# Optimization experiments

Measured on AMD Instinct MI355X. Metric: run time of the kernel, lower is better.

The kernel has to match this reference:

```python
import jax, jax.numpy as jnp
import numpy as np

N, L, C, K = 8, 16384, 256, 64  # batch, points, d_color, anchor_num; d_struct = 4*K = 256


def setup_inputs() -> dict:
    key = jax.random.key(0)
    ks = jax.random.split(key, 12)
    d_in = C + 4 * K  # 512
    s1, s2, s3 = 1.0 / np.sqrt(d_in), 1.0 / np.sqrt(128), 1.0 / np.sqrt(256)
    return {
        'feat0': jax.random.normal(ks[0], (N, L, C), jnp.float32),
        'feat1': jax.random.normal(ks[1], (N, L, C), jnp.float32),
        'pts_3d0': jax.random.normal(ks[2], (N, L, 3), jnp.float32),
        'pts_3d1': jax.random.normal(ks[3], (N, L, 3), jnp.float32),
        'anchor_i': jax.random.randint(ks[4], (N, K), 0, L, jnp.int32),
        'anchor_j': jax.random.randint(ks[5], (N, K), 0, L, jnp.int32),
        'W1': jax.random.uniform(ks[6], (d_in, 128), jnp.float32, -s1, s1),
        'b1': jax.random.uniform(ks[7], (128,), jnp.float32, -s1, s1),
        'W2': jax.random.uniform(ks[8], (128, 256), jnp.float32, -s2, s2),
        'b2': jax.random.uniform(ks[9], (256,), jnp.float32, -s2, s2),
        'W3': jax.random.uniform(ks[10], (256, C), jnp.float32, -s3, s3),
        'b3': jax.random.uniform(ks[11], (C,), jnp.float32, -s3, s3),
    }


def _structured(pts, anchor_idx):
    # pts: [N,L,3], anchor_idx: [N,K] -> [N,L,4K]
    anchors = jnp.take_along_axis(pts, anchor_idx[:, :, None], axis=1)  # [N,K,3]
    diff = pts[:, :, None, :] - anchors[:, None, :, :]                  # [N,L,K,3]
    dist = jnp.sum(diff * diff, axis=-1, keepdims=True)                 # [N,L,K,1]
    f = jnp.concatenate([diff, dist], axis=-1)                          # [N,L,K,4]
    f = f / jnp.sum(jnp.abs(f), axis=-2, keepdims=True)                 # L1 norm over K
    f = jnp.swapaxes(f, -1, -2).reshape(pts.shape[0], pts.shape[1], -1)  # [N,L,4K]
    # original l1_norm is @torch.no_grad -> structured feature is detached
    return jax.lax.stop_gradient(f)


def _mlp(x, W1, b1, W2, b2, W3, b3):
    h = jax.nn.relu(x @ W1 + b1)
    h = jax.nn.relu(h @ W2 + b2)  # dropout is identity in eval
    return h @ W3 + b3


def reference(feat0, feat1, pts_3d0, pts_3d1, anchor_i, anchor_j,
              W1, b1, W2, b2, W3, b3):
    s0 = _structured(pts_3d0, anchor_i)
    s1 = _structured(pts_3d1, anchor_j)
    aug0 = _mlp(jnp.concatenate([feat0, s0], axis=-1), W1, b1, W2, b2, W3, b3)
    aug1 = _mlp(jnp.concatenate([feat1, s1], axis=-1), W1, b1, W2, b2, W3, b3)
    return aug0, aug1
```

## Files before the change

kernel.cpp:

```cpp
#include <hip/hip_runtime.h>

typedef __bf16 bf16x8 __attribute__((ext_vector_type(8)));
typedef float f32x4 __attribute__((ext_vector_type(4)));
typedef unsigned short u16x4 __attribute__((ext_vector_type(4)));

#define NBATCH 8
#define LPTS   16384
#define CDIM   256
#define KANC   64
#define DIN    512
#define H1DIM  128
#define H2DIM  256
#define TM     64

__device__ __forceinline__ unsigned short f2b(float f){
  __bf16 h = (__bf16)f;
  return __builtin_bit_cast(unsigned short, h);
}

#define LBAR() do{ \
  asm volatile("s_waitcnt lgkmcnt(0)" ::: "memory"); \
  __builtin_amdgcn_s_barrier(); \
  asm volatile("" ::: "memory"); \
} while(0)

__global__ __launch_bounds__(256) void prep_weights(
    const float* __restrict__ W1, const float* __restrict__ W2,
    const float* __restrict__ W3, unsigned short* __restrict__ wt){
  int id = blockIdx.x * 256 + threadIdx.x;
  if (id < 65536){
    int r = id >> 9, c = id & 511;
    wt[id] = f2b(W1[c * 128 + r]);
  } else if (id < 98304){
    int t = id - 65536; int r = t >> 7, c = t & 127;
    wt[id] = f2b(W2[c * 256 + r]);
  } else if (id < 163840){
    int t = id - 98304; int r = t >> 8, c = t & 255;
    wt[id] = f2b(W3[c * 256 + r]);
  }
}

__global__ __launch_bounds__(128) void prep_coef(
    const float* __restrict__ pts0, const float* __restrict__ pts1,
    const int* __restrict__ anc_i, const int* __restrict__ anc_j,
    const float* __restrict__ W1, float* __restrict__ coef){
  const int comb = blockIdx.x;
  const int strm = comb >> 3, n = comb & 7;
  const int col  = threadIdx.x;
  __shared__ float4 anc[64];
  const float* pts  = strm ? pts1 : pts0;
  const int*   anci = strm ? anc_j : anc_i;
  if (col < 64){
    int ai = anci[n * KANC + col];
    const float* ap = pts + ((size_t)n * LPTS + ai) * 3;
    anc[col] = make_float4(ap[0], ap[1], ap[2], 0.f);
  }
  __syncthreads();
  float SX=0,CX=0,SY=0,CY=0,SZ=0,CZ=0,SD=0,ADx=0,ADy=0,ADz=0,CD2=0;
  float SAx=0,SAy=0,SAz=0,SA2=0;
  for (int k = 0; k < KANC; ++k){
    float4 a = anc[k];
    float ak2 = a.x*a.x + a.y*a.y + a.z*a.z;
    float wx = W1[(256 + k) * 128 + col];
    float wy = W1[(320 + k) * 128 + col];
    float wz = W1[(384 + k) * 128 + col];
    float wd = W1[(448 + k) * 128 + col];
    SX += wx; CX += a.x * wx;
    SY += wy; CY += a.y * wy;
    SZ += wz; CZ += a.z * wz;
    SD += wd; ADx += a.x * wd; ADy += a.y * wd; ADz += a.z * wd;
    CD2 += ak2 * wd;
    SAx += a.x; SAy += a.y; SAz += a.z; SA2 += ak2;
  }
  float* cf = coef + (size_t)comb * 12 * 128;
  cf[ 0*128+col]=SX;  cf[ 1*128+col]=CX;  cf[ 2*128+col]=SY;  cf[ 3*128+col]=CY;
  cf[ 4*128+col]=SZ;  cf[ 5*128+col]=CZ;  cf[ 6*128+col]=SD;  cf[ 7*128+col]=ADx;
  cf[ 8*128+col]=ADy; cf[ 9*128+col]=ADz; cf[10*128+col]=CD2;
  if (col == 0) cf[11*128+0] = SAx;
  if (col == 1) cf[11*128+1] = SAy;
  if (col == 2) cf[11*128+2] = SAz;
  if (col == 3) cf[11*128+3] = SA2;
}

__global__ __launch_bounds__(512, 4) void fused(
    const float* __restrict__ feat0, const float* __restrict__ feat1,
    const float* __restrict__ pts0, const float* __restrict__ pts1,
    const int* __restrict__ anc_i, const int* __restrict__ anc_j,
    const float* __restrict__ b1, const float* __restrict__ b2,
    const float* __restrict__ b3, const unsigned short* __restrict__ wt,
    const float* __restrict__ coef, float* __restrict__ out)
{
  __shared__ unsigned short xs[TM * 256];
  __shared__ unsigned short h1s[TM * H1DIM];
  __shared__ float scal[TM][12];
  unsigned short* h2s = xs;

  const int tid  = threadIdx.x;
  const int wg   = blockIdx.x;
  const int strm = wg >> 11;
  const int n    = (wg >> 8) & 7;
  const int l0   = (wg & 255) * TM;

  const float* feat = strm ? feat1 : feat0;
  const float* pts  = strm ? pts1 : pts0;
  const int*   anci = strm ? anc_j : anc_i;
  const float* cf   = coef + (size_t)((strm << 3) | n) * 12 * 128;

  const int lane = tid & 63;
  const int w    = tid >> 6;
  const int lr   = lane & 15;
  const int lg   = lane >> 4;
  const int col1 = w * 16 + lr;
  const int col0 = w * 32;
  const unsigned short* wrow1 = wt + col1 * DIN;
  const unsigned short* w2t = wt + 65536;
  const unsigned short* w3t = wt + 98304;

  float ax, ay, az;
  {
    int ai = anci[n * KANC + lane];
    const float* ap = pts + ((size_t)n * LPTS + ai) * 3;
    ax = ap[0]; ay = ap[1]; az = ap[2];
  }
  const float* pp = pts + ((size_t)n * LPTS + l0 + (tid >> 3)) * 3;
  float px = pp[0], py = pp[1], pz = pp[2];
  float SAx = cf[11*128+0], SAy = cf[11*128+1], SAz = cf[11*128+2], SA2 = cf[11*128+3];
  float cc[11];
  #pragma unroll
  for (int j = 0; j < 11; ++j) cc[j] = cf[j * 128 + col1];
  float bias1 = b1[col1];

  {
    const float4* fb = (const float4*)(feat + ((size_t)n * LPTS + l0) * CDIM);
    #pragma unroll
    for (int it = 0; it < 8; ++it){
      int flat = it * 512 + tid;
      int r = flat >> 6, c4 = flat & 63;
      float4 v = fb[flat];
      int e = (r * 256 + c4 * 4) ^ ((r & 7) << 3);
      u16x4 pk = { f2b(v.x), f2b(v.y), f2b(v.z), f2b(v.w) };
      *(u16x4*)&xs[e] = pk;
    }
  }

  {
    const int l   = tid >> 3;
    const int sub = tid & 7;
    float s0 = 0.f, s1 = 0.f, s2 = 0.f;
    #pragma unroll
    for (int i = 0; i < 8; ++i){
      int src = sub * 8 + i;
      float akx = __shfl(ax, src, 64);
      float aky = __shfl(ay, src, 64);
      float akz = __shfl(az, src, 64);
      s0 += fabsf(px - akx); s1 += fabsf(py - aky); s2 += fabsf(pz - akz);
    }
    #pragma unroll
    for (int m = 1; m <= 4; m <<= 1){
      s0 += __shfl_xor(s0, m, 64);
      s1 += __shfl_xor(s1, m, 64);
      s2 += __shfl_xor(s2, m, 64);
    }
    float pp2 = px*px + py*py + pz*pz;
    float s3 = 64.f * pp2 - 2.f * (px*SAx + py*SAy + pz*SAz) + SA2;
    float i0 = 1.f/s0, i1 = 1.f/s1, i2 = 1.f/s2, i3 = 1.f/s3;
    float u;
    switch (sub){
      case 0: u = i0 * px;       break;
      case 1: u = -i0;           break;
      case 2: u = i1 * py;       break;
      case 3: u = -i1;           break;
      case 4: u = i2 * pz;       break;
      case 5: u = -i2;           break;
      case 6: u = i3 * pp2;      break;
      default: u = -2.f*i3*px;   break;
    }
    scal[l][sub] = u;
    if (sub < 3){
      float u2 = (sub == 0) ? -2.f*i3*py : (sub == 1) ? -2.f*i3*pz : i3;
      scal[l][8 + sub] = u2;
    }
  }

  bf16x8 b1b[8];
  #pragma unroll
  for (int kk = 0; kk < 8; ++kk)
    b1b[kk] = *(const bf16x8*)&wrow1[kk * 32 + lg * 8];

  LBAR();

  {
    f32x4 acc[4] = {};
    #pragma unroll
    for (int kk = 0; kk < 8; ++kk){
      int kb = kk * 32 + lg * 8;
      #pragma unroll
      for (int m = 0; m < 4; ++m){
        int row = m * 16 + lr;
        bf16x8 a = *(const bf16x8*)&xs[(row * 256 + kb) ^ ((row & 7) << 3)];
        acc[m] = __builtin_amdgcn_mfma_f32_16x16x32_bf16(a, b1b[kk], acc[m], 0, 0, 0);
      }
    }
    #pragma unroll
    for (int m = 0; m < 4; ++m){
      #pragma unroll
      for (int r = 0; r < 4; ++r){
        int row = m * 16 + lg * 4 + r;
        f32x4 ua = *(const f32x4*)&scal[row][0];
        f32x4 ub = *(const f32x4*)&scal[row][4];
        f32x4 uc = *(const f32x4*)&scal[row][8];
        float s = acc[m][r] + bias1;
        s += ua[0]*cc[0] + ua[1]*cc[1] + ua[2]*cc[2] + ua[3]*cc[3];
        s += ub[0]*cc[4] + ub[1]*cc[5] + ub[2]*cc[6] + ub[3]*cc[7];
        s += uc[0]*cc[8] + uc[1]*cc[9] + uc[2]*cc[10];
        float v = fmaxf(s, 0.f);
        h1s[(row * H1DIM + col1) ^ ((row & 7) << 3)] = f2b(v);
      }
    }
  }

  bf16x8 b2b[8];
  #pragma unroll
  for (int kk = 0; kk < 4; ++kk){
    int kb = kk * 32 + lg * 8;
    b2b[kk * 2    ] = *(const bf16x8*)&w2t[(col0      + lr) * H1DIM + kb];
    b2b[kk * 2 + 1] = *(const bf16x8*)&w2t[(col0 + 16 + lr) * H1DIM + kb];
  }

  LBAR();

  {
    f32x4 acc[4][2] = {};
    #pragma unroll
    for (int kk = 0; kk < 4; ++kk){
      int kb = kk * 32 + lg * 8;
      #pragma unroll
      for (int m = 0; m < 4; ++m){
        int row = m * 16 + lr;
        bf16x8 a = *(const bf16x8*)&h1s[(row * H1DIM + kb) ^ ((row & 7) << 3)];
        acc[m][0] = __builtin_amdgcn_mfma_f32_16x16x32_bf16(a, b2b[kk*2  ], acc[m][0], 0, 0, 0);
        acc[m][1] = __builtin_amdgcn_mfma_f32_16x16x32_bf16(a, b2b[kk*2+1], acc[m][1], 0, 0, 0);
      }
    }
    #pragma unroll
    for (int nt = 0; nt < 2; ++nt){
      int col = col0 + nt * 16 + lr;
      float bias = b2[col];
      #pragma unroll
      for (int m = 0; m < 4; ++m){
        #pragma unroll
        for (int r = 0; r < 4; ++r){
          int row = m * 16 + lg * 4 + r;
          float v = fmaxf(acc[m][nt][r] + bias, 0.f);
          h2s[(row * H2DIM + col) ^ ((row & 7) << 3)] = f2b(v);
        }
      }
    }
  }

  bf16x8 b3b[8];
  #pragma unroll
  for (int kk = 0; kk < 4; ++kk){
    int kb = kk * 32 + lg * 8;
    b3b[kk * 2    ] = *(const bf16x8*)&w3t[(col0      + lr) * H2DIM + kb];
    b3b[kk * 2 + 1] = *(const bf16x8*)&w3t[(col0 + 16 + lr) * H2DIM + kb];
  }

  LBAR();

  {
    f32x4 acc[4][2] = {};
    #pragma unroll
    for (int kk = 0; kk < 4; ++kk){
      int kb = kk * 32 + lg * 8;
      #pragma unroll
      for (int m = 0; m < 4; ++m){
        int row = m * 16 + lr;
        bf16x8 a = *(const bf16x8*)&h2s[(row * H2DIM + kb) ^ ((row & 7) << 3)];
        acc[m][0] = __builtin_amdgcn_mfma_f32_16x16x32_bf16(a, b3b[kk*2  ], acc[m][0], 0, 0, 0);
        acc[m][1] = __builtin_amdgcn_mfma_f32_16x16x32_bf16(a, b3b[kk*2+1], acc[m][1], 0, 0, 0);
      }
    }
    #pragma unroll
    for (int kk = 0; kk < 4; ++kk){
      int kb = (kk + 4) * 32 + lg * 8;
      b3b[kk * 2    ] = *(const bf16x8*)&w3t[(col0      + lr) * H2DIM + kb];
      b3b[kk * 2 + 1] = *(const bf16x8*)&w3t[(col0 + 16 + lr) * H2DIM + kb];
    }
    #pragma unroll
    for (int kk = 0; kk < 4; ++kk){
      int kb = (kk + 4) * 32 + lg * 8;
      #pragma unroll
      for (int m = 0; m < 4; ++m){
        int row = m * 16 + lr;
        bf16x8 a = *(const bf16x8*)&h2s[(row * H2DIM + kb) ^ ((row & 7) << 3)];
        acc[m][0] = __builtin_amdgcn_mfma_f32_16x16x32_bf16(a, b3b[kk*2  ], acc[m][0], 0, 0, 0);
        acc[m][1] = __builtin_amdgcn_mfma_f32_16x16x32_bf16(a, b3b[kk*2+1], acc[m][1], 0, 0, 0);
      }
    }
    float* ob = out + (((size_t)strm * NBATCH + n) * LPTS + l0) * CDIM;
    #pragma unroll
    for (int nt = 0; nt < 2; ++nt){
      int col = col0 + nt * 16 + lr;
      float bias = b3[col];
      #pragma unroll
      for (int m = 0; m < 4; ++m){
        #pragma unroll
        for (int r = 0; r < 4; ++r){
          int row = m * 16 + lg * 4 + r;
          ob[(size_t)row * CDIM + col] = acc[m][nt][r] + bias;
        }
      }
    }
  }
}

extern "C" void kernel_launch(void* const* d_in, const int* in_sizes, int n_in,
                              void* d_out, int out_size, void* d_ws, size_t ws_size,
                              hipStream_t stream){
  const float* feat0 = (const float*)d_in[0];
  const float* feat1 = (const float*)d_in[1];
  const float* pts0  = (const float*)d_in[2];
  const float* pts1  = (const float*)d_in[3];
  const int*   anci  = (const int*)d_in[4];
  const int*   ancj  = (const int*)d_in[5];
  const float* W1    = (const float*)d_in[6];
  const float* b1    = (const float*)d_in[7];
  const float* W2    = (const float*)d_in[8];
  const float* b2    = (const float*)d_in[9];
  const float* W3    = (const float*)d_in[10];
  const float* b3    = (const float*)d_in[11];
  unsigned short* wt = (unsigned short*)d_ws;
  float* coef = (float*)((char*)d_ws + 163840 * sizeof(unsigned short));
  float* out = (float*)d_out;

  prep_weights<<<640, 256, 0, stream>>>(W1, W2, W3, wt);
  prep_coef<<<16, 128, 0, stream>>>(pts0, pts1, anci, ancj, W1, coef);
  fused<<<4096, 512, 0, stream>>>(feat0, feat1, pts0, pts1, anci, ancj,
                                  b1, b2, b3, wt, coef, out);
}
```

Before: 209.2 us.

## Load layer-1 A operand straight to registers and fold structured term into MFMA

Layer 1 no longer stages the feature tile in LDS. Each wave loads its 16 rows of features directly into bf16 MFMA A-fragments and covers a 16x64 output tile, reading the W1 B-fragments from global memory in two halves. The per-row structured-feature scalars and their precomputed coefficients are packed as bf16 with K padded to 32, so the structured contribution becomes one extra MFMA instead of scalar FMAs. h2 gets its own LDS buffer instead of aliasing the feature buffer. This removes the LDS write/read round trip for features and the scalar epilogue, at the cost of more global weight loads per wave, lower precision for the structured terms, and higher register pressure.

```diff
diff --git a/kernel.cpp b/kernel.cpp
--- a/kernel.cpp
+++ b/kernel.cpp
@@ -12,10 +12,18 @@
 #define H1DIM  128
 #define H2DIM  256
 #define TM     64
+#define USTR   40
 
 __device__ __forceinline__ unsigned short f2b(float f){
   __bf16 h = (__bf16)f;
   return __builtin_bit_cast(unsigned short, h);
+}
+
+__device__ __forceinline__ bf16x8 cvt8(float4 a, float4 b){
+  bf16x8 r;
+  r[0]=(__bf16)a.x; r[1]=(__bf16)a.y; r[2]=(__bf16)a.z; r[3]=(__bf16)a.w;
+  r[4]=(__bf16)b.x; r[5]=(__bf16)b.y; r[6]=(__bf16)b.z; r[7]=(__bf16)b.w;
+  return r;
 }
 
 #define LBAR() do{ \
@@ -43,7 +51,8 @@
 __global__ __launch_bounds__(128) void prep_coef(
     const float* __restrict__ pts0, const float* __restrict__ pts1,
     const int* __restrict__ anc_i, const int* __restrict__ anc_j,
-    const float* __restrict__ W1, float* __restrict__ coef){
+    const float* __restrict__ W1, float* __restrict__ coef,
+    unsigned short* __restrict__ cbf){
   const int comb = blockIdx.x;
   const int strm = comb >> 3, n = comb & 7;
   const int col  = threadIdx.x;
@@ -80,6 +89,12 @@
   if (col == 1) cf[11*128+1] = SAy;
   if (col == 2) cf[11*128+2] = SAz;
   if (col == 3) cf[11*128+3] = SA2;
+  unsigned short* cb = cbf + ((size_t)comb * 128 + col) * 32;
+  cb[0]=f2b(SX);  cb[1]=f2b(CX);  cb[2]=f2b(SY);  cb[3]=f2b(CY);
+  cb[4]=f2b(SZ);  cb[5]=f2b(CZ);  cb[6]=f2b(SD);  cb[7]=f2b(ADx);
+  cb[8]=f2b(ADy); cb[9]=f2b(ADz); cb[10]=f2b(CD2);
+  #pragma unroll
+  for (int j = 11; j < 32; ++j) cb[j] = 0;
 }
 
 __global__ __launch_bounds__(512, 4) void fused(
@@ -88,58 +103,57 @@
     const int* __restrict__ anc_i, const int* __restrict__ anc_j,
     const float* __restrict__ b1, const float* __restrict__ b2,
     const float* __restrict__ b3, const unsigned short* __restrict__ wt,
-    const float* __restrict__ coef, float* __restrict__ out)
+    const float* __restrict__ coef, const unsigned short* __restrict__ cbf,
+    float* __restrict__ out)
 {
-  __shared__ unsigned short xs[TM * 256];
+  __shared__ unsigned short ulds[TM * USTR];
   __shared__ unsigned short h1s[TM * H1DIM];
-  __shared__ float scal[TM][12];
-  unsigned short* h2s = xs;
+  __shared__ unsigned short h2s[TM * H2DIM];
 
   const int tid  = threadIdx.x;
   const int wg   = blockIdx.x;
   const int strm = wg >> 11;
   const int n    = (wg >> 8) & 7;
   const int l0   = (wg & 255) * TM;
+  const int comb = (strm << 3) | n;
 
   const float* feat = strm ? feat1 : feat0;
   const float* pts  = strm ? pts1 : pts0;
   const int*   anci = strm ? anc_j : anc_i;
-  const float* cf   = coef + (size_t)((strm << 3) | n) * 12 * 128;
+  const float* cf   = coef + (size_t)comb * 12 * 128;
 
   const int lane = tid & 63;
   const int w    = tid >> 6;
   const int lr   = lane & 15;
   const int lg   = lane >> 4;
-  const int col1 = w * 16 + lr;
+  const int wr   = w >> 1, wc = w & 1;
+  const int r0   = wr * 16;
   const int col0 = w * 32;
-  const unsigned short* wrow1 = wt + col1 * DIN;
   const unsigned short* w2t = wt + 65536;
   const unsigned short* w3t = wt + 98304;
+  const size_t fB = (size_t)n * LPTS;
 
   float ax, ay, az;
   {
     int ai = anci[n * KANC + lane];
-    const float* ap = pts + ((size_t)n * LPTS + ai) * 3;
+    const float* ap = pts + (fB + ai) * 3;
     ax = ap[0]; ay = ap[1]; az = ap[2];
   }
-  const float* pp = pts + ((size_t)n * LPTS + l0 + (tid >> 3)) * 3;
+  const float* pp = pts + (fB + l0 + (tid >> 3)) * 3;
   float px = pp[0], py = pp[1], pz = pp[2];
   float SAx = cf[11*128+0], SAy = cf[11*128+1], SAz = cf[11*128+2], SA2 = cf[11*128+3];
-  float cc[11];
-  #pragma unroll
-  for (int j = 0; j < 11; ++j) cc[j] = cf[j * 128 + col1];
-  float bias1 = b1[col1];
-
-  {
-    const float4* fb = (const float4*)(feat + ((size_t)n * LPTS + l0) * CDIM);
-    #pragma unroll
-    for (int it = 0; it < 8; ++it){
-      int flat = it * 512 + tid;
-      int r = flat >> 6, c4 = flat & 63;
-      float4 v = fb[flat];
-      int e = (r * 256 + c4 * 4) ^ ((r & 7) << 3);
-      u16x4 pk = { f2b(v.x), f2b(v.y), f2b(v.z), f2b(v.w) };
-      *(u16x4*)&xs[e] = pk;
+  float bias1v[4];
+  #pragma unroll
+  for (int nf = 0; nf < 4; ++nf) bias1v[nf] = b1[wc * 64 + nf * 16 + lr];
+
+  bf16x8 a1b[8];
+  {
+    const float4* fp = (const float4*)(feat + (fB + l0 + r0 + lr) * CDIM);
+    #pragma unroll
+    for (int kk = 0; kk < 8; ++kk){
+      float4 lo = fp[kk * 8 + lg * 2];
+      float4 hi = fp[kk * 8 + lg * 2 + 1];
+      a1b[kk] = cvt8(lo, hi);
     }
   }
 
@@ -164,57 +178,62 @@
     float pp2 = px*px + py*py + pz*pz;
     float s3 = 64.f * pp2 - 2.f * (px*SAx + py*SAy + pz*SAz) + SA2;
     float i0 = 1.f/s0, i1 = 1.f/s1, i2 = 1.f/s2, i3 = 1.f/s3;
-    float u;
-    switch (sub){
-      case 0: u = i0 * px;       break;
-      case 1: u = -i0;           break;
-      case 2: u = i1 * py;       break;
-      case 3: u = -i1;           break;
-      case 4: u = i2 * pz;       break;
-      case 5: u = -i2;           break;
-      case 6: u = i3 * pp2;      break;
-      default: u = -2.f*i3*px;   break;
-    }
-    scal[l][sub] = u;
-    if (sub < 3){
-      float u2 = (sub == 0) ? -2.f*i3*py : (sub == 1) ? -2.f*i3*pz : i3;
-      scal[l][8 + sub] = u2;
-    }
-  }
-
-  bf16x8 b1b[8];
-  #pragma unroll
-  for (int kk = 0; kk < 8; ++kk)
-    b1b[kk] = *(const bf16x8*)&wrow1[kk * 32 + lg * 8];
+    float a0, a1, a2, a3;
+    if (sub == 0){ a0 = i0*px;      a1 = -i0;       a2 = i1*py;  a3 = -i1; }
+    else if (sub == 1){ a0 = i2*pz; a1 = -i2;       a2 = i3*pp2; a3 = -2.f*i3*px; }
+    else if (sub == 2){ a0 = -2.f*i3*py; a1 = -2.f*i3*pz; a2 = i3; a3 = 0.f; }
+    else { a0 = a1 = a2 = a3 = 0.f; }
+    u16x4 pk = { f2b(a0), f2b(a1), f2b(a2), f2b(a3) };
+    *(u16x4*)&ulds[l * USTR + sub * 4] = pk;
+  }
+
+  bf16x8 b1b[16];
+  #pragma unroll
+  for (int kk = 0; kk < 4; ++kk){
+    #pragma unroll
+    for (int nf = 0; nf < 4; ++nf)
+      b1b[kk * 4 + nf] =
+        *(const bf16x8*)&wt[(wc * 64 + nf * 16 + lr) * DIN + kk * 32 + lg * 8];
+  }
 
   LBAR();
 
   {
     f32x4 acc[4] = {};
     #pragma unroll
-    for (int kk = 0; kk < 8; ++kk){
-      int kb = kk * 32 + lg * 8;
-      #pragma unroll
-      for (int m = 0; m < 4; ++m){
-        int row = m * 16 + lr;
-        bf16x8 a = *(const bf16x8*)&xs[(row * 256 + kb) ^ ((row & 7) << 3)];
-        acc[m] = __builtin_amdgcn_mfma_f32_16x16x32_bf16(a, b1b[kk], acc[m], 0, 0, 0);
-      }
-    }
-    #pragma unroll
-    for (int m = 0; m < 4; ++m){
+    for (int kk = 0; kk < 4; ++kk){
+      #pragma unroll
+      for (int nf = 0; nf < 4; ++nf)
+        acc[nf] = __builtin_amdgcn_mfma_f32_16x16x32_bf16(a1b[kk], b1b[kk*4+nf], acc[nf], 0, 0, 0);
+    }
+    bf16x8 b1c[16];
+    #pragma unroll
+    for (int kk = 0; kk < 4; ++kk){
+      #pragma unroll
+      for (int nf = 0; nf < 4; ++nf)
+        b1c[kk * 4 + nf] =
+          *(const bf16x8*)&wt[(wc * 64 + nf * 16 + lr) * DIN + (kk + 4) * 32 + lg * 8];
+    }
+    #pragma unroll
+    for (int kk = 0; kk < 4; ++kk){
+      #pragma unroll
+      for (int nf = 0; nf < 4; ++nf)
+        acc[nf] = __builtin_amdgcn_mfma_f32_16x16x32_bf16(a1b[kk+4], b1c[kk*4+nf], acc[nf], 0, 0, 0);
+    }
+    bf16x8 au = *(const bf16x8*)&ulds[(r0 + lr) * USTR + lg * 8];
+    #pragma unroll
+    for (int nf = 0; nf < 4; ++nf){
+      bf16x8 bcb = *(const bf16x8*)&cbf[((size_t)comb * 128 + wc * 64 + nf * 16 + lr) * 32 + lg * 8];
+      acc[nf] = __builtin_amdgcn_mfma_f32_16x16x32_bf16(au, bcb, acc[nf], 0, 0, 0);
+    }
+    #pragma unroll
+    for (int nf = 0; nf < 4; ++nf){
+      int col = wc * 64 + nf * 16 + lr;
       #pragma unroll
       for (int r = 0; r < 4; ++r){
-        int row = m * 16 + lg * 4 + r;
-        f32x4 ua = *(const f32x4*)&scal[row][0];
-        f32x4 ub = *(const f32x4*)&scal[row][4];
-        f32x4 uc = *(const f32x4*)&scal[row][8];
-        float s = acc[m][r] + bias1;
-        s += ua[0]*cc[0] + ua[1]*cc[1] + ua[2]*cc[2] + ua[3]*cc[3];
-        s += ub[0]*cc[4] + ub[1]*cc[5] + ub[2]*cc[6] + ub[3]*cc[7];
-        s += uc[0]*cc[8] + uc[1]*cc[9] + uc[2]*cc[10];
-        float v = fmaxf(s, 0.f);
-        h1s[(row * H1DIM + col1) ^ ((row & 7) << 3)] = f2b(v);
+        int row = r0 + lg * 4 + r;
+        float v = fmaxf(acc[nf][r] + bias1v[nf], 0.f);
+        h1s[(row * H1DIM + col) ^ ((row & 7) << 3)] = f2b(v);
       }
     }
   }
@@ -331,11 +350,12 @@
   const float* W3    = (const float*)d_in[10];
   const float* b3    = (const float*)d_in[11];
   unsigned short* wt = (unsigned short*)d_ws;
-  float* coef = (float*)((char*)d_ws + 163840 * sizeof(unsigned short));
+  float* coef = (float*)((char*)d_ws + 327680);
+  unsigned short* cbf = (unsigned short*)((char*)d_ws + 327680 + 98304);
   float* out = (float*)d_out;
 
   prep_weights<<<640, 256, 0, stream>>>(W1, W2, W3, wt);
-  prep_coef<<<16, 128, 0, stream>>>(pts0, pts1, anci, ancj, W1, coef);
+  prep_coef<<<16, 128, 0, stream>>>(pts0, pts1, anci, ancj, W1, coef, cbf);
   fused<<<4096, 512, 0, stream>>>(feat0, feat1, pts0, pts1, anci, ancj,
-                                  b1, b2, b3, wt, coef, out);
-}
+                                  b1, b2, b3, wt, coef, cbf, out);
+}
```

Measured after the change: 316.6 us. +51.3%, slower.

## Split fused MLP kernel into layer-1 kernel and layer-2/3 kernel via global h1

Applied to the files above, without the earlier changes.

Splits the single fused kernel into two launches. The first computes layer 1 and writes h1 in bf16 to a global workspace buffer. The second reads h1 back and runs layers 2 and 3. The aim is to cut per-kernel register and LDS pressure so more blocks fit per CU. In exchange it adds a global round trip of about 64 MB of h1 traffic plus an extra launch.

```diff
diff --git a/kernel.cpp b/kernel.cpp
--- a/kernel.cpp
+++ b/kernel.cpp
@@ -3,6 +3,7 @@
 typedef __bf16 bf16x8 __attribute__((ext_vector_type(8)));
 typedef float f32x4 __attribute__((ext_vector_type(4)));
 typedef unsigned short u16x4 __attribute__((ext_vector_type(4)));
+typedef unsigned short u16x8 __attribute__((ext_vector_type(8)));
 
 #define NBATCH 8
 #define LPTS   16384
@@ -82,39 +83,35 @@
   if (col == 3) cf[11*128+3] = SA2;
 }
 
-__global__ __launch_bounds__(512, 4) void fused(
+__global__ __launch_bounds__(512, 4) void k1(
     const float* __restrict__ feat0, const float* __restrict__ feat1,
     const float* __restrict__ pts0, const float* __restrict__ pts1,
     const int* __restrict__ anc_i, const int* __restrict__ anc_j,
-    const float* __restrict__ b1, const float* __restrict__ b2,
-    const float* __restrict__ b3, const unsigned short* __restrict__ wt,
-    const float* __restrict__ coef, float* __restrict__ out)
+    const float* __restrict__ b1, const unsigned short* __restrict__ wt,
+    const float* __restrict__ coef, unsigned short* __restrict__ h1g)
 {
   __shared__ unsigned short xs[TM * 256];
   __shared__ unsigned short h1s[TM * H1DIM];
   __shared__ float scal[TM][12];
-  unsigned short* h2s = xs;
 
   const int tid  = threadIdx.x;
   const int wg   = blockIdx.x;
   const int strm = wg >> 11;
   const int n    = (wg >> 8) & 7;
   const int l0   = (wg & 255) * TM;
+  const int comb = (strm << 3) | n;
 
   const float* feat = strm ? feat1 : feat0;
   const float* pts  = strm ? pts1 : pts0;
   const int*   anci = strm ? anc_j : anc_i;
-  const float* cf   = coef + (size_t)((strm << 3) | n) * 12 * 128;
+  const float* cf   = coef + (size_t)comb * 12 * 128;
 
   const int lane = tid & 63;
   const int w    = tid >> 6;
   const int lr   = lane & 15;
   const int lg   = lane >> 4;
   const int col1 = w * 16 + lr;
-  const int col0 = w * 32;
   const unsigned short* wrow1 = wt + col1 * DIN;
-  const unsigned short* w2t = wt + 65536;
-  const unsigned short* w3t = wt + 98304;
 
   float ax, ay, az;
   {
@@ -219,6 +216,59 @@
     }
   }
 
+  LBAR();
+
+  {
+    unsigned short* hg = h1g + ((size_t)comb * LPTS + l0) * H1DIM;
+    #pragma unroll
+    for (int it = 0; it < 2; ++it){
+      int flat = it * 512 + tid;
+      int row = flat >> 4, c8 = flat & 15;
+      int off = row * H1DIM + c8 * 8;
+      u16x8 v = *(const u16x8*)&h1s[off ^ ((row & 7) << 3)];
+      *(u16x8*)&hg[off] = v;
+    }
+  }
+}
+
+__global__ __launch_bounds__(512, 4) void k23(
+    const unsigned short* __restrict__ h1g,
+    const float* __restrict__ b2, const float* __restrict__ b3,
+    const unsigned short* __restrict__ wt, float* __restrict__ out)
+{
+  __shared__ unsigned short h1s[TM * H1DIM];
+  __shared__ unsigned short h2s[TM * H2DIM];
+
+  const int tid  = threadIdx.x;
+  const int wg   = blockIdx.x;
+  const int strm = wg >> 11;
+  const int n    = (wg >> 8) & 7;
+  const int l0   = (wg & 255) * TM;
+  const int comb = (strm << 3) | n;
+
+  const int lane = tid & 63;
+  const int w    = tid >> 6;
+  const int lr   = lane & 15;
+  const int lg   = lane >> 4;
+  const int col0 = w * 32;
+  const unsigned short* w2t = wt + 65536;
+  const unsigned short* w3t = wt + 98304;
+
+  float bias2a = b2[col0 + lr], bias2b = b2[col0 + 16 + lr];
+  float bias3a = b3[col0 + lr], bias3b = b3[col0 + 16 + lr];
+
+  {
+    const unsigned short* hg = h1g + ((size_t)comb * LPTS + l0) * H1DIM;
+    #pragma unroll
+    for (int it = 0; it < 2; ++it){
+      int flat = it * 512 + tid;
+      int row = flat >> 4, c8 = flat & 15;
+      int off = row * H1DIM + c8 * 8;
+      u16x8 v = *(const u16x8*)&hg[off];
+      *(u16x8*)&h1s[off ^ ((row & 7) << 3)] = v;
+    }
+  }
+
   bf16x8 b2b[8];
   #pragma unroll
   for (int kk = 0; kk < 4; ++kk){
@@ -244,8 +294,8 @@
     }
     #pragma unroll
     for (int nt = 0; nt < 2; ++nt){
+      float bias = nt ? bias2b : bias2a;
       int col = col0 + nt * 16 + lr;
-      float bias = b2[col];
       #pragma unroll
       for (int m = 0; m < 4; ++m){
         #pragma unroll
@@ -301,8 +351,8 @@
     float* ob = out + (((size_t)strm * NBATCH + n) * LPTS + l0) * CDIM;
     #pragma unroll
     for (int nt = 0; nt < 2; ++nt){
+      float bias = nt ? bias3b : bias3a;
       int col = col0 + nt * 16 + lr;
-      float bias = b3[col];
       #pragma unroll
       for (int m = 0; m < 4; ++m){
         #pragma unroll
@@ -331,11 +381,13 @@
   const float* W3    = (const float*)d_in[10];
   const float* b3    = (const float*)d_in[11];
   unsigned short* wt = (unsigned short*)d_ws;
-  float* coef = (float*)((char*)d_ws + 163840 * sizeof(unsigned short));
+  float* coef = (float*)((char*)d_ws + 327680);
+  unsigned short* h1g = (unsigned short*)((char*)d_ws + 327680 + 98304);
   float* out = (float*)d_out;
 
   prep_weights<<<640, 256, 0, stream>>>(W1, W2, W3, wt);
   prep_coef<<<16, 128, 0, stream>>>(pts0, pts1, anci, ancj, W1, coef);
-  fused<<<4096, 512, 0, stream>>>(feat0, feat1, pts0, pts1, anci, ancj,
-                                  b1, b2, b3, wt, coef, out);
-}
+  k1<<<4096, 512, 0, stream>>>(feat0, feat1, pts0, pts1, anci, ancj,
+                               b1, wt, coef, h1g);
+  k23<<<4096, 512, 0, stream>>>(h1g, b2, b3, wt, out);
+}
```

New measurement: 221.0 us. +5.7%, slower.
